# Kernel optimization log

Measured on AMD Instinct MI355X. Metric: run time of the kernel, lower is better.

The kernel has to match this reference:

```python
import jax, jax.numpy as jnp
import numpy as np

S = 4096       # sequence length
D = 1024       # d_model
H = 16         # heads
DK = 64        # d_k == d_v
VERY_SMOL_NUM = -1e9


def setup_inputs() -> dict:
    key = jax.random.key(0)
    ks = jax.random.split(key, 14)
    sd = 1.0 / np.sqrt(D)
    inp = {
        "V": jax.random.normal(ks[0], (S, D), jnp.float32),
        "K": jax.random.normal(ks[1], (S, D), jnp.float32),
        "Q": jax.random.normal(ks[2], (S, D), jnp.float32),
        # per-head projection weights, stored [in, out] (x @ W + b)
        "WQ": jax.random.normal(ks[3], (H, D, DK), jnp.float32) * sd,
        "bQ": jax.random.normal(ks[4], (H, DK), jnp.float32) * sd,
        "WK": jax.random.normal(ks[5], (H, D, DK), jnp.float32) * sd,
        "bK": jax.random.normal(ks[6], (H, DK), jnp.float32) * sd,
        "WV": jax.random.normal(ks[7], (H, D, DK), jnp.float32) * sd,
        "bV": jax.random.normal(ks[8], (H, DK), jnp.float32) * sd,
        "WO": jax.random.normal(ks[9], (D, D), jnp.float32) * sd,
        "bO": jax.random.normal(ks[10], (D,), jnp.float32) * sd,
    }
    return inp


def reference(V, K, Q, WQ, bQ, WK, bK, WV, bV, WO, bO):
    # per-head projections, vectorized over heads: [H, S, DK]
    q = jnp.einsum('sd,hdk->hsk', Q, WQ) + bQ[:, None, :]
    k = jnp.einsum('sd,hdk->hsk', K, WK) + bK[:, None, :]
    v = jnp.einsum('sd,hdk->hsk', V, WV) + bV[:, None, :]
    # full QK^T per head, scaled
    scores = jnp.einsum('hsk,htk->hst', q, k) / jnp.sqrt(jnp.float32(DK))
    # original bug faithfully preserved: with masked=True the causal additive
    # mask (triu(ones,1) * VERY_SMOL_NUM) is applied TWICE
    tri = jnp.triu(jnp.ones((S, S), jnp.float32), 1) * VERY_SMOL_NUM
    scores = scores + 2.0 * tri
    # torch Softmax(dim=1) on 2D [S,S] scores == softmax over keys (last dim)
    attn = jax.nn.softmax(scores, axis=-1)
    heads = jnp.einsum('hst,htv->hsv', attn, v)          # [H, S, DK]
    cat = heads.transpose(1, 0, 2).reshape(S, H * DK)    # concat over heads
    return cat @ WO + bO
```

## Files before the change

### kernel.cpp

```cpp
#include <hip/hip_runtime.h>

typedef unsigned short u16;
typedef unsigned int u32;
typedef __attribute__((ext_vector_type(8))) __bf16 bf16x8;
typedef __attribute__((ext_vector_type(4))) float f32x4;
typedef __attribute__((ext_vector_type(16))) float f32x16;

#define S_LEN 4096
#define D_MODEL 1024
#define NH 16
#define DHEAD 64

__device__ __forceinline__ u16 f2bf(float f){
  unsigned u = __float_as_uint(f);
  u += 0x7FFFu + ((u >> 16) & 1u);
  return (u16)(u >> 16);
}

__device__ __forceinline__ void gload_lds16(const void* g, void* l){
  __builtin_amdgcn_global_load_lds((const __attribute__((address_space(1))) void*)g,
                                   (__attribute__((address_space(3))) void*)l, 16, 0, 0);
}

__device__ __forceinline__ void xcd_decode(int bid, int& bm, int& bn){
  int xcd = bid & 7, w = bid >> 3;
  bm = ((xcd << 2) | (w >> 3)) * 128;
  bn = (w & 7) * 128;
}

__global__ __launch_bounds__(256) void cvt3_kernel(const float* __restrict__ q,
                                                   const float* __restrict__ k,
                                                   const float* __restrict__ v,
                                                   u16* __restrict__ oq,
                                                   u16* __restrict__ ok,
                                                   u16* __restrict__ ov){
  int z = blockIdx.y;
  const float* in = (z==0)? q : (z==1)? k : v;
  u16* out = (z==0)? oq : (z==1)? ok : ov;
  int i = blockIdx.x*256 + threadIdx.x;
  float4 w = reinterpret_cast<const float4*>(in)[i];
  ushort4 o;
  o.x = f2bf(w.x); o.y = f2bf(w.y); o.z = f2bf(w.z); o.w = f2bf(w.w);
  reinterpret_cast<ushort4*>(out)[i] = o;
}

__global__ __launch_bounds__(256) void tcvt_all_kernel(const float* __restrict__ wq,
                                                       const float* __restrict__ wk,
                                                       const float* __restrict__ wv,
                                                       const float* __restrict__ wo,
                                                       u16* __restrict__ oq,
                                                       u16* __restrict__ ok,
                                                       u16* __restrict__ ov,
                                                       u16* __restrict__ oo){
  __shared__ float tile[64][67];
  int y = blockIdx.y, z = blockIdx.z, x = blockIdx.x;
  int r0 = x*64, c0;
  const float* in; u16* out; int inStride;
  if (y < 3){
    in  = ((y==0)? wq : (y==1)? wk : wv) + (size_t)z*1024*64;
    out = ((y==0)? oq : (y==1)? ok : ov) + (size_t)z*1024*64;
    c0 = 0; inStride = 64;
  } else {
    in = wo; out = oo; c0 = z*64; inStride = 1024;
  }
  int tid = threadIdx.x;
  #pragma unroll
  for (int c=0;c<4;c++){
    int cl = c*256 + tid;
    int row = cl >> 4, cc = (cl & 15) * 4;
    float4 v = *reinterpret_cast<const float4*>(in + (size_t)(r0+row)*inStride + c0 + cc);
    tile[row][cc+0]=v.x; tile[row][cc+1]=v.y; tile[row][cc+2]=v.z; tile[row][cc+3]=v.w;
  }
  __syncthreads();
  #pragma unroll
  for (int c=0;c<4;c++){
    int cl = c*256 + tid;
    int crow = cl >> 4, rc = (cl & 15) * 4;
    ushort4 o;
    o.x = f2bf(tile[rc+0][crow]);
    o.y = f2bf(tile[rc+1][crow]);
    o.z = f2bf(tile[rc+2][crow]);
    o.w = f2bf(tile[rc+3][crow]);
    *reinterpret_cast<ushort4*>(out + (size_t)(c0+crow)*1024 + r0 + rc) = o;
  }
}

__global__ __launch_bounds__(512) void gemm_qkv_kernel(
    const u16* __restrict__ Qb, const u16* __restrict__ Kb, const u16* __restrict__ Vb,
    const u16* __restrict__ WtQ, const u16* __restrict__ WtK, const u16* __restrict__ WtV,
    const float* __restrict__ bQ, const float* __restrict__ bK, const float* __restrict__ bV,
    u16* __restrict__ qbuf, u16* __restrict__ kbuf, u16* __restrict__ vtb, float qscale){
  const int M = S_LEN, N = D_MODEL, K = D_MODEL;
  int z = blockIdx.z;
  const u16* A  = (z==0)? Qb  : (z==1)? Kb  : Vb;
  const u16* Bt = (z==0)? WtQ : (z==1)? WtK : WtV;
  const float* bias = (z==0)? bQ : (z==1)? bK : bV;
  float oscale = (z==0)? qscale : 1.0f;

  __shared__ __align__(16) unsigned char lsA[2][16384];
  __shared__ __align__(16) unsigned char lsB[2][16384];
  int tid = threadIdx.x;
  int bm, bn;
  xcd_decode(blockIdx.x, bm, bn);
  int wave = tid >> 6, lane = tid & 63;
  int wm = (wave >> 1) * 32, wn = (wave & 1) * 64;
  int lrow = lane & 15, lgrp = lane >> 4;

  f32x4 acc[2][4] = {};

  auto STAGE = [&](int buf, int k0){
    #pragma unroll
    for (int c=0;c<4;c++){
      int id = c*512 + tid;
      int r = (id & 1023) >> 3;
      int kc = id & 7;
      int cs = (kc ^ (r & 7)) << 3;
      if (id < 1024)
        gload_lds16(A + (size_t)(bm+r)*K + k0 + cs, lsA[buf] + ((id & 1023) << 4));
      else
        gload_lds16(Bt + (size_t)(bn+r)*K + k0 + cs, lsB[buf] + ((id & 1023) << 4));
    }
  };

  STAGE(0, 0);
  int cur = 0;
  for (int k0 = 0; k0 < K; k0 += 64){
    __syncthreads();
    if (k0 + 64 < K) STAGE(cur^1, k0 + 64);
    #pragma unroll
    for (int ks=0;ks<2;ks++){
      bf16x8 af[2], bfr[4];
      #pragma unroll
      for (int i=0;i<2;i++){
        int ar = wm + i*16 + lrow;
        af[i] = *reinterpret_cast<const bf16x8*>(lsA[cur] + ((ar*128 + ks*64 + lgrp*16) ^ ((ar&7)<<4)));
      }
      #pragma unroll
      for (int j=0;j<4;j++){
        int br = wn + j*16 + lrow;
        bfr[j] = *reinterpret_cast<const bf16x8*>(lsB[cur] + ((br*128 + ks*64 + lgrp*16) ^ ((br&7)<<4)));
      }
      __builtin_amdgcn_s_setprio(1);
      #pragma unroll
      for (int i=0;i<2;i++)
        #pragma unroll
        for (int j=0;j<4;j++)
          acc[i][j] = __builtin_amdgcn_mfma_f32_16x16x32_bf16(af[i], bfr[j], acc[i][j], 0,0,0);
      __builtin_amdgcn_s_setprio(0);
    }
    cur ^= 1;
  }

  #pragma unroll
  for (int j=0;j<4;j++){
    int n = bn + wn + j*16 + lrow;
    float bv = bias[n];
    int hh = n >> 6, kk = n & 63;
    #pragma unroll
    for (int i=0;i<2;i++){
      int m0 = bm + wm + i*16 + lgrp*4;
      float v[4];
      #pragma unroll
      for (int r=0;r<4;r++) v[r] = (acc[i][j][r] + bv) * oscale;
      if (z < 2){
        u16* o = (z==0)? qbuf : kbuf;
        #pragma unroll
        for (int r=0;r<4;r++) o[((size_t)hh*M + m0 + r)*64 + kk] = f2bf(v[r]);
      } else {
        ushort4 p; p.x=f2bf(v[0]); p.y=f2bf(v[1]); p.z=f2bf(v[2]); p.w=f2bf(v[3]);
        *reinterpret_cast<ushort4*>(vtb + ((size_t)hh*64 + kk)*M + m0) = p;
      }
    }
  }
}

__global__ __launch_bounds__(512) void gemm_out_kernel(const u16* __restrict__ A,
                                                       const u16* __restrict__ Bt,
                                                       const float* __restrict__ bias,
                                                       float* __restrict__ dst,
                                                       int M, int N, int K){
  __shared__ __align__(16) unsigned char lsA[2][16384];
  __shared__ __align__(16) unsigned char lsB[2][16384];
  int tid = threadIdx.x;
  int bm, bn;
  xcd_decode(blockIdx.x, bm, bn);
  int wave = tid >> 6, lane = tid & 63;
  int wm = (wave >> 1) * 32, wn = (wave & 1) * 64;
  int lrow = lane & 15, lgrp = lane >> 4;

  f32x4 acc[2][4] = {};

  auto STAGE = [&](int buf, int k0){
    #pragma unroll
    for (int c=0;c<4;c++){
      int id = c*512 + tid;
      int r = (id & 1023) >> 3;
      int kc = id & 7;
      int cs = (kc ^ (r & 7)) << 3;
      if (id < 1024)
        gload_lds16(A + (size_t)(bm+r)*K + k0 + cs, lsA[buf] + ((id & 1023) << 4));
      else
        gload_lds16(Bt + (size_t)(bn+r)*K + k0 + cs, lsB[buf] + ((id & 1023) << 4));
    }
  };

  STAGE(0, 0);
  int cur = 0;
  for (int k0 = 0; k0 < K; k0 += 64){
    __syncthreads();
    if (k0 + 64 < K) STAGE(cur^1, k0 + 64);
    #pragma unroll
    for (int ks=0;ks<2;ks++){
      bf16x8 af[2], bfr[4];
      #pragma unroll
      for (int i=0;i<2;i++){
        int ar = wm + i*16 + lrow;
        af[i] = *reinterpret_cast<const bf16x8*>(lsA[cur] + ((ar*128 + ks*64 + lgrp*16) ^ ((ar&7)<<4)));
      }
      #pragma unroll
      for (int j=0;j<4;j++){
        int br = wn + j*16 + lrow;
        bfr[j] = *reinterpret_cast<const bf16x8*>(lsB[cur] + ((br*128 + ks*64 + lgrp*16) ^ ((br&7)<<4)));
      }
      __builtin_amdgcn_s_setprio(1);
      #pragma unroll
      for (int i=0;i<2;i++)
        #pragma unroll
        for (int j=0;j<4;j++)
          acc[i][j] = __builtin_amdgcn_mfma_f32_16x16x32_bf16(af[i], bfr[j], acc[i][j], 0,0,0);
      __builtin_amdgcn_s_setprio(0);
    }
    cur ^= 1;
  }

  #pragma unroll
  for (int j=0;j<4;j++){
    int n = bn + wn + j*16 + lrow;
    float bv = bias[n];
    #pragma unroll
    for (int i=0;i<2;i++){
      int m0 = bm + wm + i*16 + lgrp*4;
      #pragma unroll
      for (int r=0;r<4;r++) dst[(size_t)(m0+r)*N + n] = acc[i][j][r] + bv;
    }
  }
}

__global__ __launch_bounds__(512, 2) void flash_attn_kernel(const u16* __restrict__ qb,
                                                            const u16* __restrict__ kb,
                                                            const u16* __restrict__ vtb,
                                                            u16* __restrict__ pO,
                                                            float2* __restrict__ pml){
  int b = blockIdx.x;
  int h = b & 15;
  int u = b >> 4;
  int qt = 15 - (u >> 2);
  int quarter = u & 3;
  int seg = qt + 1;
  int j0 = quarter * seg, j1 = j0 + seg;

  int tid = threadIdx.x, wave = tid >> 6, lane = tid & 63;
  int l31 = lane & 31, hi = lane >> 5;
  const u16* qh  = qb  + (size_t)h * S_LEN * 64;
  const u16* kh  = kb  + (size_t)h * S_LEN * 64;
  const u16* vth = vtb + (size_t)h * 64 * S_LEN;

  __shared__ __align__(16) unsigned char lsK[2][8192];
  __shared__ __align__(16) unsigned char lsV[2][8192];

  int qw = qt*256 + wave*32;

  bf16x8 qf[4];
  #pragma unroll
  for (int ks=0;ks<4;ks++)
    qf[ks] = *reinterpret_cast<const bf16x8*>(qh + (size_t)(qw + l31)*64 + ks*16 + hi*8);

  f32x16 oacc0 = {}, oacc1 = {};
  float m_run = -3e38f, l_run = 0.f;

  const int kvbase = hi*1024 + l31*16;
  const int krow = tid & 63, kcol = (tid >> 6) << 3;

  auto STAGE = [&](int buf, int jj){
    int kv0 = jj*64;
    gload_lds16(kh + (size_t)(kv0 + krow)*64 + kcol, lsK[buf] + (tid << 4));
    gload_lds16(vth + (size_t)krow*S_LEN + kv0 + kcol, lsV[buf] + (tid << 4));
  };

  STAGE(0, j0);
  int cur = 0;
  for (int j = j0; j < j1; j++){
    __syncthreads();
    if (j + 1 < j1) STAGE(cur^1, j + 1);

    int kv0 = j*64;
    int rel0 = qw - kv0;
    int rel1 = rel0 - 32;
    if (rel0 >= 0){
      bool act1 = rel1 >= 0;
      const unsigned char* Kc = lsK[cur] + kvbase;
      const unsigned char* Vc = lsV[cur] + kvbase;

      f32x16 s0 = {}, s1 = {};
      __builtin_amdgcn_s_setprio(1);
      #pragma unroll
      for (int ks=0;ks<4;ks++){
        bf16x8 kf = *reinterpret_cast<const bf16x8*>(Kc + ks*2048);
        s0 = __builtin_amdgcn_mfma_f32_32x32x16_bf16(kf, qf[ks], s0, 0,0,0);
      }
      if (act1){
        #pragma unroll
        for (int ks=0;ks<4;ks++){
          bf16x8 kf = *reinterpret_cast<const bf16x8*>(Kc + ks*2048 + 512);
          s1 = __builtin_amdgcn_mfma_f32_32x32x16_bf16(kf, qf[ks], s1, 0,0,0);
        }
      }
      __builtin_amdgcn_s_setprio(0);

      if (rel0 == 0){
        #pragma unroll
        for (int reg=0;reg<16;reg++){
          int kvloc = (reg & 3) + 8*(reg >> 2) + 4*hi;
          if (kvloc > l31) s0[reg] = -3e38f;
        }
      }
      if (act1 && rel1 == 0){
        #pragma unroll
        for (int reg=0;reg<16;reg++){
          int kvloc = (reg & 3) + 8*(reg >> 2) + 4*hi;
          if (kvloc > l31) s1[reg] = -3e38f;
        }
      }

      float tm[8];
      #pragma unroll
      for (int i=0;i<8;i++) tm[i] = fmaxf(s0[i], s0[i+8]);
      if (act1){
        #pragma unroll
        for (int i=0;i<8;i++) tm[i] = fmaxf(tm[i], fmaxf(s1[i], s1[i+8]));
      }
      #pragma unroll
      for (int st=4; st>=1; st>>=1){
        #pragma unroll
        for (int i=0;i<st;i++) tm[i] = fmaxf(tm[i], tm[i+st]);
      }
      float mx = fmaxf(tm[0], __shfl_xor(tm[0], 32));

      if (!__all(mx <= m_run + 11.54f)){
        float mnew = fmaxf(m_run, mx);
        float al = __builtin_amdgcn_exp2f(m_run - mnew);
        m_run = mnew; l_run *= al;
        #pragma unroll
        for (int reg=0;reg<16;reg++){ oacc0[reg] *= al; oacc1[reg] *= al; }
      }

      #pragma unroll
      for (int reg=0;reg<16;reg++) s0[reg] = __builtin_amdgcn_exp2f(s0[reg] - m_run);
      if (act1){
        #pragma unroll
        for (int reg=0;reg<16;reg++) s1[reg] = __builtin_amdgcn_exp2f(s1[reg] - m_run);
      }
      float tp[8];
      #pragma unroll
      for (int i=0;i<8;i++) tp[i] = s0[i] + s0[i+8];
      if (act1){
        #pragma unroll
        for (int i=0;i<8;i++) tp[i] += s1[i] + s1[i+8];
      }
      #pragma unroll
      for (int st=4; st>=1; st>>=1){
        #pragma unroll
        for (int i=0;i<st;i++) tp[i] += tp[i+st];
      }
      l_run += tp[0] + __shfl_xor(tp[0], 32);

      #pragma unroll
      for (int b01=0;b01<2;b01++){
        u32 A,B,C,D;
        asm("v_cvt_pk_bf16_f32 %0, %1, %2" : "=v"(A) : "v"(s0[8*b01+0]), "v"(s0[8*b01+1]));
        asm("v_cvt_pk_bf16_f32 %0, %1, %2" : "=v"(B) : "v"(s0[8*b01+2]), "v"(s0[8*b01+3]));
        asm("v_cvt_pk_bf16_f32 %0, %1, %2" : "=v"(C) : "v"(s0[8*b01+4]), "v"(s0[8*b01+5]));
        asm("v_cvt_pk_bf16_f32 %0, %1, %2" : "=v"(D) : "v"(s0[8*b01+6]), "v"(s0[8*b01+7]));
        asm("v_permlane32_swap_b32 %0, %1" : "+v"(A), "+v"(C));
        asm("v_permlane32_swap_b32 %0, %1" : "+v"(B), "+v"(D));
        union { u32 w[4]; bf16x8 v; } U;
        U.w[0]=A; U.w[1]=B; U.w[2]=C; U.w[3]=D;
        bf16x8 vf0 = *reinterpret_cast<const bf16x8*>(Vc + b01*2048);
        bf16x8 vf1 = *reinterpret_cast<const bf16x8*>(Vc + b01*2048 + 512);
        __builtin_amdgcn_s_setprio(1);
        oacc0 = __builtin_amdgcn_mfma_f32_32x32x16_bf16(vf0, U.v, oacc0, 0,0,0);
        oacc1 = __builtin_amdgcn_mfma_f32_32x32x16_bf16(vf1, U.v, oacc1, 0,0,0);
        __builtin_amdgcn_s_setprio(0);
      }
      if (act1){
        #pragma unroll
        for (int b01=0;b01<2;b01++){
          u32 A,B,C,D;
          asm("v_cvt_pk_bf16_f32 %0, %1, %2" : "=v"(A) : "v"(s1[8*b01+0]), "v"(s1[8*b01+1]));
          asm("v_cvt_pk_bf16_f32 %0, %1, %2" : "=v"(B) : "v"(s1[8*b01+2]), "v"(s1[8*b01+3]));
          asm("v_cvt_pk_bf16_f32 %0, %1, %2" : "=v"(C) : "v"(s1[8*b01+4]), "v"(s1[8*b01+5]));
          asm("v_cvt_pk_bf16_f32 %0, %1, %2" : "=v"(D) : "v"(s1[8*b01+6]), "v"(s1[8*b01+7]));
          asm("v_permlane32_swap_b32 %0, %1" : "+v"(A), "+v"(C));
          asm("v_permlane32_swap_b32 %0, %1" : "+v"(B), "+v"(D));
          union { u32 w[4]; bf16x8 v; } U;
          U.w[0]=A; U.w[1]=B; U.w[2]=C; U.w[3]=D;
          bf16x8 vf0 = *reinterpret_cast<const bf16x8*>(Vc + (2+b01)*2048);
          bf16x8 vf1 = *reinterpret_cast<const bf16x8*>(Vc + (2+b01)*2048 + 512);
          __builtin_amdgcn_s_setprio(1);
          oacc0 = __builtin_amdgcn_mfma_f32_32x32x16_bf16(vf0, U.v, oacc0, 0,0,0);
          oacc1 = __builtin_amdgcn_mfma_f32_32x32x16_bf16(vf1, U.v, oacc1, 0,0,0);
          __builtin_amdgcn_s_setprio(0);
        }
      }
    }
    cur ^= 1;
  }

  int q = qw + l31;
  if (hi == 0){
    float2 ml; ml.x = m_run; ml.y = l_run;
    pml[((size_t)quarter*NH + h)*S_LEN + q] = ml;
  }
  #pragma unroll
  for (int df=0;df<2;df++){
    #pragma unroll
    for (int q4=0;q4<4;q4++){
      float a0 = df ? oacc1[4*q4+0] : oacc0[4*q4+0];
      float a1 = df ? oacc1[4*q4+1] : oacc0[4*q4+1];
      float a2 = df ? oacc1[4*q4+2] : oacc0[4*q4+2];
      float a3 = df ? oacc1[4*q4+3] : oacc0[4*q4+3];
      u32 w0d, w1d;
      asm("v_cvt_pk_bf16_f32 %0, %1, %2" : "=v"(w0d) : "v"(a0), "v"(a1));
      asm("v_cvt_pk_bf16_f32 %0, %1, %2" : "=v"(w1d) : "v"(a2), "v"(a3));
      int dquad = df*8 + 2*q4 + hi;
      uint2 pv; pv.x = w0d; pv.y = w1d;
      *reinterpret_cast<uint2*>(pO + (((size_t)(quarter*NH + h)*16 + dquad)*S_LEN + q)*4) = pv;
    }
  }
}

__global__ __launch_bounds__(256) void combine_kernel(const u16* __restrict__ pO,
                                                      const float2* __restrict__ pml,
                                                      u16* __restrict__ catb){
  int tid = threadIdx.x;
  int dq = tid & 15, qo = tid >> 4;
  int h = blockIdx.y;
  int q = blockIdx.x*16 + qo;
  float2 ml[4];
  #pragma unroll
  for (int i=0;i<4;i++) ml[i] = pml[((size_t)i*NH + h)*S_LEN + q];
  float m = fmaxf(fmaxf(ml[0].x, ml[1].x), fmaxf(ml[2].x, ml[3].x));
  float w[4], denom = 0.f;
  #pragma unroll
  for (int i=0;i<4;i++){ w[i] = __builtin_amdgcn_exp2f(ml[i].x - m); denom += w[i]*ml[i].y; }
  float inv = 1.0f / denom;
  float x0=0.f, x1=0.f, x2=0.f, x3=0.f;
  #pragma unroll
  for (int i=0;i<4;i++){
    ushort4 a = reinterpret_cast<const ushort4*>(pO)[((size_t)i*NH*16 + (size_t)h*16 + dq)*S_LEN + q];
    x0 += __uint_as_float((u32)a.x << 16) * w[i];
    x1 += __uint_as_float((u32)a.y << 16) * w[i];
    x2 += __uint_as_float((u32)a.z << 16) * w[i];
    x3 += __uint_as_float((u32)a.w << 16) * w[i];
  }
  ushort4 o;
  o.x = f2bf(x0*inv); o.y = f2bf(x1*inv); o.z = f2bf(x2*inv); o.w = f2bf(x3*inv);
  *reinterpret_cast<ushort4*>(catb + (size_t)q*D_MODEL + h*64 + dq*4) = o;
}

extern "C" void kernel_launch(void* const* d_in, const int* in_sizes, int n_in,
                              void* d_out, int out_size, void* d_ws, size_t ws_size,
                              hipStream_t stream){
  (void)in_sizes; (void)n_in; (void)out_size; (void)ws_size;
  const float* V  = (const float*)d_in[0];
  const float* Km = (const float*)d_in[1];
  const float* Q  = (const float*)d_in[2];
  const float* WQ = (const float*)d_in[3];
  const float* bQ = (const float*)d_in[4];
  const float* WK = (const float*)d_in[5];
  const float* bK = (const float*)d_in[6];
  const float* WV = (const float*)d_in[7];
  const float* bV = (const float*)d_in[8];
  const float* WO = (const float*)d_in[9];
  const float* bO = (const float*)d_in[10];
  float* out = (float*)d_out;

  char* ws = (char*)d_ws;
  const size_t SZ_SD = (size_t)S_LEN * D_MODEL * 2;
  const size_t SZ_W  = (size_t)D_MODEL * D_MODEL * 2;
  u16* Qb   = (u16*)(ws);
  u16* Kb   = (u16*)(ws + SZ_SD);
  u16* Vb   = (u16*)(ws + 2*SZ_SD);
  u16* WtQ  = (u16*)(ws + 3*SZ_SD);
  u16* WtK  = (u16*)(ws + 3*SZ_SD + SZ_W);
  u16* WtV  = (u16*)(ws + 3*SZ_SD + 2*SZ_W);
  u16* WtO  = (u16*)(ws + 3*SZ_SD + 3*SZ_W);
  u16* qbuf = (u16*)(ws + 3*SZ_SD + 4*SZ_W);
  u16* kbuf = (u16*)(ws + 4*SZ_SD + 4*SZ_W);
  u16* vtb  = (u16*)(ws + 5*SZ_SD + 4*SZ_W);
  u16* catb = (u16*)(ws + 6*SZ_SD + 4*SZ_W);
  u16* pO   = (u16*)(ws + 7*SZ_SD + 4*SZ_W);
  float2* pml = (float2*)(ws + 11*SZ_SD + 4*SZ_W);

  const float QSCALE = 0.18033688011112042f;

  cvt3_kernel<<<dim3(4096,3),256,0,stream>>>(Q, Km, V, Qb, Kb, Vb);
  tcvt_all_kernel<<<dim3(16,4,16),256,0,stream>>>(WQ, WK, WV, WO, WtQ, WtK, WtV, WtO);
  gemm_qkv_kernel<<<dim3(256,1,3),512,0,stream>>>(Qb, Kb, Vb, WtQ, WtK, WtV,
                                                  bQ, bK, bV, qbuf, kbuf, vtb, QSCALE);
  flash_attn_kernel<<<dim3(1024),512,0,stream>>>(qbuf, kbuf, vtb, pO, pml);
  combine_kernel<<<dim3(256,16),256,0,stream>>>(pO, pml, catb);
  gemm_out_kernel<<<dim3(256),512,0,stream>>>(catb, WtO, bO, out, S_LEN, D_MODEL, D_MODEL);
}
```

Before: 139.9 us.

## Pair long and short causal query tiles per flash-attention block for balanced work

Each flash-attention block now processes two query tiles, a long one (15-p) and its complementary short one (p), covering a quarter of each tile's KV range, so every block runs exactly 17 KV steps. The grid is halved from 1024 to 512 blocks, and the epilogue runs once per tile, with Q fragments and accumulators reset between tiles. The aim is to remove the load imbalance of causal tiles with different lengths. The cost is fewer blocks, which may lower occupancy or GPU fill, and a mid-loop epilogue that adds register pressure.

After: 153.4 us. +9.6%, slower.

```diff
diff --git a/kernel.cpp b/kernel.cpp
--- a/kernel.cpp
+++ b/kernel.cpp
@@ -253,11 +253,11 @@
                                                             float2* __restrict__ pml){
   int b = blockIdx.x;
   int h = b & 15;
-  int u = b >> 4;
-  int qt = 15 - (u >> 2);
-  int quarter = u & 3;
-  int seg = qt + 1;
-  int j0 = quarter * seg, j1 = j0 + seg;
+  int pi = b >> 4;
+  int p = pi >> 2, c = pi & 3;
+  int qtA = 15 - p, qtB = p;
+  int segA = 16 - p, segB = p + 1;
+  int jA0 = c * segA, jB0 = c * segB;
 
   int tid = threadIdx.x, wave = tid >> 6, lane = tid & 63;
   int l31 = lane & 31, hi = lane >> 5;
@@ -268,6 +268,7 @@
   __shared__ __align__(16) unsigned char lsK[2][8192];
   __shared__ __align__(16) unsigned char lsV[2][8192];
 
+  int qt = qtA;
   int qw = qt*256 + wave*32;
 
   bf16x8 qf[4];
@@ -280,6 +281,8 @@
 
   const int kvbase = hi*1024 + l31*16;
   const int krow = tid & 63, kcol = (tid >> 6) << 3;
+
+  auto jof = [&](int t){ return (t < segA) ? (jA0 + t) : (jB0 + t - segA); };
 
   auto STAGE = [&](int buf, int jj){
     int kv0 = jj*64;
@@ -287,13 +290,37 @@
     gload_lds16(vth + (size_t)krow*S_LEN + kv0 + kcol, lsV[buf] + (tid << 4));
   };
 
-  STAGE(0, j0);
+  auto EPILOGUE = [&](){
+    int q = qw + l31;
+    if (hi == 0){
+      float2 ml; ml.x = m_run; ml.y = l_run;
+      pml[((size_t)c*NH + h)*S_LEN + q] = ml;
+    }
+    #pragma unroll
+    for (int df=0;df<2;df++){
+      #pragma unroll
+      for (int q4=0;q4<4;q4++){
+        float a0 = df ? oacc1[4*q4+0] : oacc0[4*q4+0];
+        float a1 = df ? oacc1[4*q4+1] : oacc0[4*q4+1];
+        float a2 = df ? oacc1[4*q4+2] : oacc0[4*q4+2];
+        float a3 = df ? oacc1[4*q4+3] : oacc0[4*q4+3];
+        u32 w0d, w1d;
+        asm("v_cvt_pk_bf16_f32 %0, %1, %2" : "=v"(w0d) : "v"(a0), "v"(a1));
+        asm("v_cvt_pk_bf16_f32 %0, %1, %2" : "=v"(w1d) : "v"(a2), "v"(a3));
+        int dquad = df*8 + 2*q4 + hi;
+        uint2 pv; pv.x = w0d; pv.y = w1d;
+        *reinterpret_cast<uint2*>(pO + (((size_t)(c*NH + h)*16 + dquad)*S_LEN + q)*4) = pv;
+      }
+    }
+  };
+
+  STAGE(0, jof(0));
   int cur = 0;
-  for (int j = j0; j < j1; j++){
+  for (int t = 0; t < 17; t++){
     __syncthreads();
-    if (j + 1 < j1) STAGE(cur^1, j + 1);
-
-    int kv0 = j*64;
+    if (t + 1 < 17) STAGE(cur^1, jof(t + 1));
+
+    int kv0 = jof(t)*64;
     int rel0 = qw - kv0;
     int rel1 = rel0 - 32;
     if (rel0 >= 0){
@@ -413,29 +440,20 @@
         }
       }
     }
+
+    if (t == segA - 1 || t == 16){
+      EPILOGUE();
+      if (t == segA - 1){
+        qt = qtB;
+        qw = qt*256 + wave*32;
+        #pragma unroll
+        for (int ks=0;ks<4;ks++)
+          qf[ks] = *reinterpret_cast<const bf16x8*>(qh + (size_t)(qw + l31)*64 + ks*16 + hi*8);
+        oacc0 = f32x16{}; oacc1 = f32x16{};
+        m_run = -3e38f; l_run = 0.f;
+      }
+    }
     cur ^= 1;
-  }
-
-  int q = qw + l31;
-  if (hi == 0){
-    float2 ml; ml.x = m_run; ml.y = l_run;
-    pml[((size_t)quarter*NH + h)*S_LEN + q] = ml;
-  }
-  #pragma unroll
-  for (int df=0;df<2;df++){
-    #pragma unroll
-    for (int q4=0;q4<4;q4++){
-      float a0 = df ? oacc1[4*q4+0] : oacc0[4*q4+0];
-      float a1 = df ? oacc1[4*q4+1] : oacc0[4*q4+1];
-      float a2 = df ? oacc1[4*q4+2] : oacc0[4*q4+2];
-      float a3 = df ? oacc1[4*q4+3] : oacc0[4*q4+3];
-      u32 w0d, w1d;
-      asm("v_cvt_pk_bf16_f32 %0, %1, %2" : "=v"(w0d) : "v"(a0), "v"(a1));
-      asm("v_cvt_pk_bf16_f32 %0, %1, %2" : "=v"(w1d) : "v"(a2), "v"(a3));
-      int dquad = df*8 + 2*q4 + hi;
-      uint2 pv; pv.x = w0d; pv.y = w1d;
-      *reinterpret_cast<uint2*>(pO + (((size_t)(quarter*NH + h)*16 + dquad)*S_LEN + q)*4) = pv;
-    }
   }
 }
 
@@ -508,7 +526,7 @@
   tcvt_all_kernel<<<dim3(16,4,16),256,0,stream>>>(WQ, WK, WV, WO, WtQ, WtK, WtV, WtO);
   gemm_qkv_kernel<<<dim3(256,1,3),512,0,stream>>>(Qb, Kb, Vb, WtQ, WtK, WtV,
                                                   bQ, bK, bV, qbuf, kbuf, vtb, QSCALE);
-  flash_attn_kernel<<<dim3(1024),512,0,stream>>>(qbuf, kbuf, vtb, pO, pml);
+  flash_attn_kernel<<<dim3(512),512,0,stream>>>(qbuf, kbuf, vtb, pO, pml);
   combine_kernel<<<dim3(256,16),256,0,stream>>>(pO, pml, catb);
   gemm_out_kernel<<<dim3(256),512,0,stream>>>(catb, WtO, bO, out, S_LEN, D_MODEL, D_MODEL);
 }
```
